# Kernel optimization log

Hardware: AMD Instinct MI355X
Metric: run time of the kernel (lower is better)

Reference implementation:

```python
import jax, jax.numpy as jnp
import numpy as np

N_NODES = 50000
HEADS = 4
NEG_SLOPE = 0.2


def _gat_conv(x, src, dst, W, a_src, a_dst, b):
    """PyG GATConv (concat=True, add_self_loops already applied to src/dst).
    x: [N, F_in], W: [F_in, H*C], a_src/a_dst: [H, C], b: [H*C]."""
    N = x.shape[0]
    HC = W.shape[1]
    C = HC // HEADS
    h = (x @ W).reshape(N, HEADS, C)                       # [N, H, C]
    alpha_s = (h * a_src[None]).sum(-1)                    # [N, H]
    alpha_d = (h * a_dst[None]).sum(-1)                    # [N, H]
    e = jax.nn.leaky_relu(alpha_s[src] + alpha_d[dst], NEG_SLOPE)  # [E, H]
    # segment softmax over incoming edges of each destination node
    m = jax.ops.segment_max(e, dst, num_segments=N)        # [N, H]
    ex = jnp.exp(e - m[dst])
    denom = jax.ops.segment_sum(ex, dst, num_segments=N)   # [N, H]
    alpha = ex / (denom[dst] + 1e-16)                      # [E, H]
    msg = h[src] * alpha[:, :, None]                       # [E, H, C]
    out = jax.ops.segment_sum(msg, dst, num_segments=N)    # [N, H, C]
    return out.reshape(N, HC) + b


def _glorot(key, shape, fan):
    lim = float(np.sqrt(6.0 / fan))
    return jax.random.uniform(key, shape, jnp.float32, -lim, lim)


def setup_inputs() -> dict:
    key = jax.random.key(0)
    ks = jax.random.split(key, 16)
    N, E, F_in, Hid, Out = N_NODES, 800000, 128, 256, 256
    x = jax.random.normal(ks[0], (N, F_in), jnp.float32)
    edge_index = jax.random.randint(ks[1], (2, E), 0, N, jnp.int64)
    C1, C2, C3 = Hid // HEADS, Hid // HEADS, Out // HEADS
    d = {"x": x, "edge_index": edge_index}
    dims = [(F_in, HEADS * C1, C1), (Hid, HEADS * C2, C2), (Hid, HEADS * C3, C3)]
    for i, (fi, fo, c) in enumerate(dims, 1):
        d[f"W{i}"] = _glorot(ks[3 * i], (fi, fo), fi + fo)
        d[f"a_src{i}"] = _glorot(ks[3 * i + 1], (HEADS, c), HEADS * c)
        d[f"a_dst{i}"] = _glorot(ks[3 * i + 2], (HEADS, c), HEADS * c)
        d[f"b{i}"] = jnp.zeros((fo,), jnp.float32)
    return d


def reference(x, edge_index, W1, a_src1, a_dst1, b1, W2, a_src2, a_dst2, b2, W3, a_src3, a_dst3, b3):
    N = x.shape[0]
    loops = jnp.arange(N, dtype=edge_index.dtype)
    src = jnp.concatenate([edge_index[0], loops])  # PyG add_self_loops=True
    dst = jnp.concatenate([edge_index[1], loops])
    h = _gat_conv(x, src, dst, W1, a_src1, a_dst1, b1)
    h = jax.nn.relu(h)  # dropout inert in eval mode
    h = _gat_conv(h, src, dst, W2, a_src2, a_dst2, b2)
    h = jax.nn.relu(h)
    return _gat_conv(h, src, dst, W3, a_src3, a_dst3, b3)
```

## Files before the change

### kernel.cpp

```cpp
#include <hip/hip_runtime.h>
#include <hip/hip_bf16.h>

typedef unsigned short u16;
typedef __attribute__((ext_vector_type(8))) short short8;
typedef __attribute__((ext_vector_type(4))) float f32x4;

#define HC 256
#define NHEAD 4

__device__ __forceinline__ u16 f2b_rne(float v) {
  __hip_bfloat16 b = __float2bfloat16(v);
  union { __hip_bfloat16 b; u16 u; } cv; cv.b = b; return cv.u;
}

__global__ void convert_w(const float* __restrict__ W, u16* __restrict__ Wth,
                          u16* __restrict__ Wtl, int K) {
  int id = blockIdx.x * 256 + threadIdx.x;
  if (id >= K * 256) return;
  int k = id >> 8, n = id & 255;
  float v = W[id];
  unsigned bits = __float_as_uint(v);
  u16 hi = (u16)(bits >> 16);
  float hf = __uint_as_float((unsigned)hi << 16);
  u16 lo = f2b_rne(v - hf);
  Wth[n * K + k] = hi;
  Wtl[n * K + k] = lo;
}

#define GBM 128
#define GBN 128
#define GBK 64

__global__ __launch_bounds__(256, 2) void gemm_mfma(
    const float* __restrict__ A, const u16* __restrict__ Bth,
    const u16* __restrict__ Btl, float* __restrict__ C, int M, int K) {
  __shared__ u16 AH[128 * 64], AL[128 * 64], BH[128 * 64], BL[128 * 64];
  const int tid = threadIdx.x;
  const int lane = tid & 63;
  const int wave = tid >> 6;
  const int wm = (wave & 1) * 64;
  const int wn = (wave >> 1) * 64;
  const int bm = blockIdx.x * GBM;
  const int bn = blockIdx.y * GBN;

  const int srow = tid >> 1;
  const int skh  = (tid & 1) * 32;

  f32x4 acc[4][4] = {};

  const int agm = (bm + srow < M) ? (bm + srow) : (M - 1);

  for (int bk = 0; bk < K; bk += GBK) {
    float4 a0[4], a1[4];
    const float* arow = A + (size_t)agm * K + bk + skh;
#pragma unroll
    for (int u = 0; u < 4; ++u) {
      a0[u] = ((const float4*)arow)[2 * u];
      a1[u] = ((const float4*)arow)[2 * u + 1];
    }
    short8 sbh[4], sbl[4];
    const u16* bhrow = Bth + (size_t)(bn + srow) * K + bk + skh;
    const u16* blrow = Btl + (size_t)(bn + srow) * K + bk + skh;
#pragma unroll
    for (int u = 0; u < 4; ++u) {
      sbh[u] = *(const short8*)(bhrow + 8 * u);
      sbl[u] = *(const short8*)(blrow + 8 * u);
    }
    __syncthreads();
#pragma unroll
    for (int u = 0; u < 4; ++u) {
      int idx = (srow * 64 + skh + u * 8) ^ ((srow & 7) << 3);
      float va[8] = {a0[u].x, a0[u].y, a0[u].z, a0[u].w,
                     a1[u].x, a1[u].y, a1[u].z, a1[u].w};
      short8 hi, lo;
#pragma unroll
      for (int j = 0; j < 8; ++j) {
        unsigned bits = __float_as_uint(va[j]);
        u16 h = (u16)(bits >> 16);
        float hf = __uint_as_float((unsigned)h << 16);
        u16 l = f2b_rne(va[j] - hf);
        ((short*)&hi)[j] = (short)h;
        ((short*)&lo)[j] = (short)l;
      }
      *(short8*)&AH[idx] = hi;
      *(short8*)&AL[idx] = lo;
      *(short8*)&BH[idx] = sbh[u];
      *(short8*)&BL[idx] = sbl[u];
    }
    __syncthreads();
#pragma unroll
    for (int ks = 0; ks < 2; ++ks) {
      const int k0 = ks * 32 + (lane >> 4) * 8;
      short8 fah[4], fal[4], fbh[4], fbl[4];
#pragma unroll
      for (int mt = 0; mt < 4; ++mt) {
        int r = wm + mt * 16 + (lane & 15);
        int idx = (r * 64 + k0) ^ ((r & 7) << 3);
        fah[mt] = *(const short8*)&AH[idx];
        fal[mt] = *(const short8*)&AL[idx];
      }
#pragma unroll
      for (int nt = 0; nt < 4; ++nt) {
        int r = wn + nt * 16 + (lane & 15);
        int idx = (r * 64 + k0) ^ ((r & 7) << 3);
        fbh[nt] = *(const short8*)&BH[idx];
        fbl[nt] = *(const short8*)&BL[idx];
      }
#pragma unroll
      for (int mt = 0; mt < 4; ++mt)
#pragma unroll
        for (int nt = 0; nt < 4; ++nt) {
          acc[mt][nt] = __builtin_amdgcn_mfma_f32_16x16x32_bf16(
              fbh[nt], fah[mt], acc[mt][nt], 0, 0, 0);
          acc[mt][nt] = __builtin_amdgcn_mfma_f32_16x16x32_bf16(
              fbh[nt], fal[mt], acc[mt][nt], 0, 0, 0);
          acc[mt][nt] = __builtin_amdgcn_mfma_f32_16x16x32_bf16(
              fbl[nt], fah[mt], acc[mt][nt], 0, 0, 0);
        }
    }
  }
#pragma unroll
  for (int mt = 0; mt < 4; ++mt) {
    int row = bm + wm + mt * 16 + (lane & 15);
    if (row < M) {
      float* cp = C + (size_t)row * HC + bn + wn + (lane >> 4) * 4;
#pragma unroll
      for (int nt = 0; nt < 4; ++nt)
        *(f32x4*)(cp + nt * 16) = acc[mt][nt];
    }
  }
}

__global__ __launch_bounds__(256) void alpha_kernel(
    const float* __restrict__ h, const float* __restrict__ a_src,
    const float* __restrict__ a_dst, float* __restrict__ as_g,
    float* __restrict__ ad_g, int N) {
  const int wave = threadIdx.x >> 6;
  const int lane = threadIdx.x & 63;
  const int n = blockIdx.x * 4 + wave;
  if (n >= N) return;
  float4 hv = ((const float4*)h)[(size_t)n * 64 + lane];
  float4 s4 = ((const float4*)a_src)[lane];
  float4 d4 = ((const float4*)a_dst)[lane];
  float ps = hv.x * s4.x + hv.y * s4.y + hv.z * s4.z + hv.w * s4.w;
  float pd = hv.x * d4.x + hv.y * d4.y + hv.z * d4.z + hv.w * d4.w;
#pragma unroll
  for (int off = 1; off < 16; off <<= 1) {
    ps += __shfl_xor(ps, off);
    pd += __shfl_xor(pd, off);
  }
  if ((lane & 15) == 0) {
    int head = lane >> 4;
    as_g[n * NHEAD + head] = ps;
    ad_g[n * NHEAD + head] = pd;
  }
}

__device__ __forceinline__ float comp4(float4 v, int i) {
  return (i == 0) ? v.x : (i == 1) ? v.y : (i == 2) ? v.z : v.w;
}

__global__ __launch_bounds__(256) void aggregate_kernel(
    const float* __restrict__ h, const float* __restrict__ as_g,
    const float* __restrict__ ad_g, const int* __restrict__ row_ptr,
    const int* __restrict__ csr_src, const float* __restrict__ bias,
    float* __restrict__ out, int relu_flag, int N) {
  const int wave = threadIdx.x >> 6;
  const int lane = threadIdx.x & 63;
  const int n = blockIdx.x * 4 + wave;
  if (n >= N) return;
  const int head = lane >> 4;
  const float4* __restrict__ h4 = (const float4*)h;
  const float4* __restrict__ as4 = (const float4*)as_g;

  const int beg = row_ptr[n];
  const int end = row_ptr[n + 1];

  float4 m4 = make_float4(-1e30f, -1e30f, -1e30f, -1e30f);
  for (int j = beg + lane; j < end; j += 64) {
    float4 a = as4[csr_src[j]];
    m4.x = fmaxf(m4.x, a.x); m4.y = fmaxf(m4.y, a.y);
    m4.z = fmaxf(m4.z, a.z); m4.w = fmaxf(m4.w, a.w);
  }
#pragma unroll
  for (int off = 32; off > 0; off >>= 1) {
    m4.x = fmaxf(m4.x, __shfl_xor(m4.x, off));
    m4.y = fmaxf(m4.y, __shfl_xor(m4.y, off));
    m4.z = fmaxf(m4.z, __shfl_xor(m4.z, off));
    m4.w = fmaxf(m4.w, __shfl_xor(m4.w, off));
  }
  const float ad = comp4(((const float4*)ad_g)[n], head);
  float mm = ad + comp4(m4, head);
  mm = (mm >= 0.f) ? mm : 0.2f * mm;

  float l = 0.f;
  float4 acc = make_float4(0.f, 0.f, 0.f, 0.f);
  for (int j0 = beg; j0 < end; j0 += 8) {
    int s[8];
    float ae[8];
    float4 hv[8];
#pragma unroll
    for (int u = 0; u < 8; ++u) {
      int j = j0 + u;
      s[u] = csr_src[(j < end) ? j : (end - 1)];
    }
#pragma unroll
    for (int u = 0; u < 8; ++u) ae[u] = as_g[s[u] * NHEAD + head];
#pragma unroll
    for (int u = 0; u < 8; ++u) hv[u] = h4[(size_t)s[u] * 64 + lane];
#pragma unroll
    for (int u = 0; u < 8; ++u) {
      float e = ae[u] + ad;
      e = (e >= 0.f) ? e : 0.2f * e;
      float p = __expf(e - mm);
      p = (j0 + u < end) ? p : 0.f;
      l += p;
      acc.x = fmaf(p, hv[u].x, acc.x);
      acc.y = fmaf(p, hv[u].y, acc.y);
      acc.z = fmaf(p, hv[u].z, acc.z);
      acc.w = fmaf(p, hv[u].w, acc.w);
    }
  }
  const float inv = 1.f / (l + 1e-16f);
  float4 b4 = ((const float4*)bias)[lane];
  float4 o;
  o.x = acc.x * inv + b4.x; o.y = acc.y * inv + b4.y;
  o.z = acc.z * inv + b4.z; o.w = acc.w * inv + b4.w;
  if (relu_flag) {
    o.x = fmaxf(o.x, 0.f); o.y = fmaxf(o.y, 0.f);
    o.z = fmaxf(o.z, 0.f); o.w = fmaxf(o.w, 0.f);
  }
  ((float4*)out)[(size_t)n * 64 + lane] = o;
}

__global__ void detect_kernel(const int* __restrict__ ei32, int* flag) {
  const int t = threadIdx.x;
  int bad = 0;
#pragma unroll
  for (int r = 0; r < 4; ++r) {
    int i = r * 64 + t;
    if (ei32[2 * i + 1] != 0) bad = 1;
  }
#pragma unroll
  for (int off = 32; off > 0; off >>= 1) bad |= __shfl_down(bad, off);
  if (t == 0) *flag = bad ? 0 : 1;
}

__device__ inline void edge_pair(const int* __restrict__ ei32,
                                 const long long* __restrict__ ei64, int is64,
                                 int e, int E, int& src, int& dst) {
  if (e < E) {
    if (is64) { src = (int)ei64[e]; dst = (int)ei64[(size_t)E + e]; }
    else      { src = ei32[e];      dst = ei32[(size_t)E + e]; }
  } else {
    src = dst = e - E;
  }
}

__global__ void count_kernel(const int* __restrict__ ei32, const int* __restrict__ flag,
                             int* __restrict__ cnt, int E, int Nn) {
  int e = blockIdx.x * blockDim.x + threadIdx.x;
  if (e >= E + Nn) return;
  int is64 = *flag;
  int src, dst;
  edge_pair(ei32, (const long long*)ei32, is64, e, E, src, dst);
  atomicAdd(&cnt[dst], 1);
}

__global__ void scatter_kernel(const int* __restrict__ ei32, const int* __restrict__ flag,
                               int* __restrict__ cursor, int* __restrict__ csr_src,
                               int E, int Nn) {
  int e = blockIdx.x * blockDim.x + threadIdx.x;
  if (e >= E + Nn) return;
  int is64 = *flag;
  int src, dst;
  edge_pair(ei32, (const long long*)ei32, is64, e, E, src, dst);
  int pos = atomicAdd(&cursor[dst], 1);
  csr_src[pos] = src;
}

__global__ __launch_bounds__(256) void scan_blocks(
    const int* __restrict__ cnt, int* __restrict__ local,
    int* __restrict__ partials, int Nn) {
  __shared__ int swave[4];
  const int t = threadIdx.x, lane = t & 63, w = t >> 6;
  const int idx = blockIdx.x * 256 + t;
  int v = (idx < Nn) ? cnt[idx] : 0;
  int x = v;
#pragma unroll
  for (int off = 1; off < 64; off <<= 1) {
    int y = __shfl_up(x, off);
    if (lane >= off) x += y;
  }
  if (lane == 63) swave[w] = x;
  __syncthreads();
  int wofs = 0;
#pragma unroll
  for (int i = 0; i < 3; ++i) wofs += (i < w) ? swave[i] : 0;
  if (idx < Nn) local[idx] = wofs + x - v;
  if (t == 255) partials[blockIdx.x] = wofs + x;
}

__global__ __launch_bounds__(256) void scan_partials(
    int* __restrict__ partials, int nb, int* __restrict__ total_out) {
  __shared__ int swave[4];
  const int t = threadIdx.x, lane = t & 63, w = t >> 6;
  int v = (t < nb) ? partials[t] : 0;
  int x = v;
#pragma unroll
  for (int off = 1; off < 64; off <<= 1) {
    int y = __shfl_up(x, off);
    if (lane >= off) x += y;
  }
  if (lane == 63) swave[w] = x;
  __syncthreads();
  int wofs = 0;
#pragma unroll
  for (int i = 0; i < 3; ++i) wofs += (i < w) ? swave[i] : 0;
  int excl = wofs + x - v;
  if (t < nb) partials[t] = excl;
  if (t == nb - 1) *total_out = excl + v;
}

__global__ void add_offsets(const int* __restrict__ local,
                            const int* __restrict__ partials,
                            int* __restrict__ row_ptr, int* __restrict__ cursor,
                            int Nn) {
  const int idx = blockIdx.x * 256 + threadIdx.x;
  if (idx < Nn) {
    int v = local[idx] + partials[blockIdx.x];
    row_ptr[idx] = v;
    cursor[idx] = v;
  }
}

static inline size_t align_up(size_t v) { return (v + 255) & ~(size_t)255; }

extern "C" void kernel_launch(void* const* d_in, const int* in_sizes, int n_in,
                              void* d_out, int out_size, void* d_ws, size_t ws_size,
                              hipStream_t stream) {
  const float* x      = (const float*)d_in[0];
  const int*   ei32   = (const int*)d_in[1];
  const float* W1     = (const float*)d_in[2];
  const float* asrc1  = (const float*)d_in[3];
  const float* adst1  = (const float*)d_in[4];
  const float* b1     = (const float*)d_in[5];
  const float* W2     = (const float*)d_in[6];
  const float* asrc2  = (const float*)d_in[7];
  const float* adst2  = (const float*)d_in[8];
  const float* b2     = (const float*)d_in[9];
  const float* W3     = (const float*)d_in[10];
  const float* asrc3  = (const float*)d_in[11];
  const float* adst3  = (const float*)d_in[12];
  const float* b3     = (const float*)d_in[13];

  const int N = in_sizes[0] / 128;
  const int E = in_sizes[1] / 2;
  const int ET = E + N;
  float* out = (float*)d_out;
  const int nb = (N + 255) / 256;

  char* w = (char*)d_ws;
  float* H       = (float*)w; w += align_up((size_t)N * HC * sizeof(float));
  float* AS      = (float*)w; w += align_up((size_t)N * NHEAD * sizeof(float));
  float* AD      = (float*)w; w += align_up((size_t)N * NHEAD * sizeof(float));
  int*   cnt     = (int*)w;   w += align_up((size_t)N * sizeof(int));
  int*   local   = (int*)w;   w += align_up((size_t)N * sizeof(int));
  int*   row_ptr = (int*)w;   w += align_up((size_t)(N + 1) * sizeof(int));
  int*   cursor  = (int*)w;   w += align_up((size_t)(N + 1) * sizeof(int));
  int*   parts   = (int*)w;   w += align_up(256 * sizeof(int));
  int*   csr_src = (int*)w;   w += align_up((size_t)ET * sizeof(int));
  u16*   Wth     = (u16*)w;   w += align_up((size_t)256 * 256 * sizeof(u16));
  u16*   Wtl     = (u16*)w;   w += align_up((size_t)256 * 256 * sizeof(u16));
  int*   flag    = (int*)w;   w += align_up(sizeof(int));

  hipMemsetAsync(cnt, 0, (size_t)N * sizeof(int), stream);
  detect_kernel<<<1, 64, 0, stream>>>(ei32, flag);
  count_kernel<<<(ET + 255) / 256, 256, 0, stream>>>(ei32, flag, cnt, E, N);
  scan_blocks<<<nb, 256, 0, stream>>>(cnt, local, parts, N);
  scan_partials<<<1, 256, 0, stream>>>(parts, nb, row_ptr + N);
  add_offsets<<<nb, 256, 0, stream>>>(local, parts, row_ptr, cursor, N);
  scatter_kernel<<<(ET + 255) / 256, 256, 0, stream>>>(ei32, flag, cursor, csr_src, E, N);

  const dim3 gemm_grid((N + GBM - 1) / GBM, HC / GBN);
  const int ablk = (N + 3) / 4;

  convert_w<<<(128 * 256 + 255) / 256, 256, 0, stream>>>(W1, Wth, Wtl, 128);
  gemm_mfma<<<gemm_grid, 256, 0, stream>>>(x, Wth, Wtl, H, N, 128);
  alpha_kernel<<<ablk, 256, 0, stream>>>(H, asrc1, adst1, AS, AD, N);
  aggregate_kernel<<<ablk, 256, 0, stream>>>(H, AS, AD, row_ptr, csr_src, b1, out, 1, N);

  convert_w<<<(256 * 256 + 255) / 256, 256, 0, stream>>>(W2, Wth, Wtl, 256);
  gemm_mfma<<<gemm_grid, 256, 0, stream>>>(out, Wth, Wtl, H, N, 256);
  alpha_kernel<<<ablk, 256, 0, stream>>>(H, asrc2, adst2, AS, AD, N);
  aggregate_kernel<<<ablk, 256, 0, stream>>>(H, AS, AD, row_ptr, csr_src, b2, out, 1, N);

  convert_w<<<(256 * 256 + 255) / 256, 256, 0, stream>>>(W3, Wth, Wtl, 256);
  gemm_mfma<<<gemm_grid, 256, 0, stream>>>(out, Wth, Wtl, H, N, 256);
  alpha_kernel<<<ablk, 256, 0, stream>>>(H, asrc3, adst3, AS, AD, N);
  aggregate_kernel<<<ablk, 256, 0, stream>>>(H, AS, AD, row_ptr, csr_src, b3, out, 0, N);
}
```

Before: 611.8 us.

## Split softmax edge weights into separate kernel and use two waves per node

Moves the per-edge exp/leaky-relu softmax weight computation and normalizer into a new edge_weights kernel that writes weights to a workspace buffer. The aggregation kernel then uses two waves per destination node, each covering alternating chunks of 8 edges, and combines their partial sums through shared memory. This targets latency in the gather loop by doubling the memory-level parallelism per node. In exchange it adds an extra kernel launch per layer and an extra write and read of an E×4 float weight buffer, plus a block-wide synchronisation.

```diff
diff --git a/kernel.cpp b/kernel.cpp
--- a/kernel.cpp
+++ b/kernel.cpp
@@ -160,19 +160,17 @@
   return (i == 0) ? v.x : (i == 1) ? v.y : (i == 2) ? v.z : v.w;
 }
 
-__global__ __launch_bounds__(256) void aggregate_kernel(
-    const float* __restrict__ h, const float* __restrict__ as_g,
-    const float* __restrict__ ad_g, const int* __restrict__ row_ptr,
-    const int* __restrict__ csr_src, const float* __restrict__ bias,
-    float* __restrict__ out, int relu_flag, int N) {
+__global__ __launch_bounds__(256) void edge_weights(
+    const float* __restrict__ as_g, const float* __restrict__ ad_g,
+    const int* __restrict__ row_ptr, const int* __restrict__ csr_src,
+    float* __restrict__ w_buf, float* __restrict__ inv_l, int N) {
   const int wave = threadIdx.x >> 6;
   const int lane = threadIdx.x & 63;
   const int n = blockIdx.x * 4 + wave;
   if (n >= N) return;
   const int head = lane >> 4;
-  const float4* __restrict__ h4 = (const float4*)h;
+  const int sub = lane & 15;
   const float4* __restrict__ as4 = (const float4*)as_g;
-
   const int beg = row_ptr[n];
   const int end = row_ptr[n + 1];
 
@@ -193,44 +191,82 @@
   float mm = ad + comp4(m4, head);
   mm = (mm >= 0.f) ? mm : 0.2f * mm;
 
-  float l = 0.f;
+  float lsum = 0.f;
+  for (int j0 = beg; j0 < end; j0 += 16) {
+    int j = j0 + sub;
+    int jc = (j < end) ? j : (end - 1);
+    int s = csr_src[jc];
+    float e = as_g[s * NHEAD + head] + ad;
+    e = (e >= 0.f) ? e : 0.2f * e;
+    float w = __expf(e - mm);
+    w_buf[(size_t)jc * NHEAD + head] = w;
+    lsum += (j < end) ? w : 0.f;
+  }
+#pragma unroll
+  for (int off = 1; off < 16; off <<= 1) lsum += __shfl_xor(lsum, off);
+  if (sub == 0) inv_l[n * NHEAD + head] = 1.f / (lsum + 1e-16f);
+}
+
+__global__ __launch_bounds__(512, 4) void aggregate_kernel(
+    const float* __restrict__ h, const float* __restrict__ w_buf,
+    const float* __restrict__ inv_l, const int* __restrict__ row_ptr,
+    const int* __restrict__ csr_src, const float* __restrict__ bias,
+    float* __restrict__ out, int relu_flag, int N) {
+  __shared__ float4 lacc[4][64];
+  const int wave = threadIdx.x >> 6;
+  const int lane = threadIdx.x & 63;
+  const int p = wave >> 1;
+  const int q = wave & 1;
+  const int n = blockIdx.x * 4 + p;
+  const int nc = (n < N) ? n : (N - 1);
+  const int head = lane >> 4;
+  const float4* __restrict__ h4 = (const float4*)h;
+
+  const int beg = row_ptr[nc];
+  const int end = row_ptr[nc + 1];
+
   float4 acc = make_float4(0.f, 0.f, 0.f, 0.f);
-  for (int j0 = beg; j0 < end; j0 += 8) {
-    int s[8];
-    float ae[8];
+  for (int j0 = beg + q * 8; j0 < end; j0 += 16) {
+    int jc[8];
+    float wv[8];
     float4 hv[8];
 #pragma unroll
     for (int u = 0; u < 8; ++u) {
       int j = j0 + u;
-      s[u] = csr_src[(j < end) ? j : (end - 1)];
-    }
-#pragma unroll
-    for (int u = 0; u < 8; ++u) ae[u] = as_g[s[u] * NHEAD + head];
-#pragma unroll
-    for (int u = 0; u < 8; ++u) hv[u] = h4[(size_t)s[u] * 64 + lane];
+      jc[u] = (j < end) ? j : (end - 1);
+    }
+    int sv[8];
+#pragma unroll
+    for (int u = 0; u < 8; ++u) sv[u] = csr_src[jc[u]];
+#pragma unroll
+    for (int u = 0; u < 8; ++u) wv[u] = w_buf[(size_t)jc[u] * NHEAD + head];
+#pragma unroll
+    for (int u = 0; u < 8; ++u) hv[u] = h4[(size_t)sv[u] * 64 + lane];
 #pragma unroll
     for (int u = 0; u < 8; ++u) {
-      float e = ae[u] + ad;
-      e = (e >= 0.f) ? e : 0.2f * e;
-      float p = __expf(e - mm);
-      p = (j0 + u < end) ? p : 0.f;
-      l += p;
-      acc.x = fmaf(p, hv[u].x, acc.x);
-      acc.y = fmaf(p, hv[u].y, acc.y);
-      acc.z = fmaf(p, hv[u].z, acc.z);
-      acc.w = fmaf(p, hv[u].w, acc.w);
-    }
-  }
-  const float inv = 1.f / (l + 1e-16f);
-  float4 b4 = ((const float4*)bias)[lane];
-  float4 o;
-  o.x = acc.x * inv + b4.x; o.y = acc.y * inv + b4.y;
-  o.z = acc.z * inv + b4.z; o.w = acc.w * inv + b4.w;
-  if (relu_flag) {
-    o.x = fmaxf(o.x, 0.f); o.y = fmaxf(o.y, 0.f);
-    o.z = fmaxf(o.z, 0.f); o.w = fmaxf(o.w, 0.f);
-  }
-  ((float4*)out)[(size_t)n * 64 + lane] = o;
+      float wm = (j0 + u < end) ? wv[u] : 0.f;
+      acc.x = fmaf(wm, hv[u].x, acc.x);
+      acc.y = fmaf(wm, hv[u].y, acc.y);
+      acc.z = fmaf(wm, hv[u].z, acc.z);
+      acc.w = fmaf(wm, hv[u].w, acc.w);
+    }
+  }
+  if (q == 1) lacc[p][lane] = acc;
+  __syncthreads();
+  if (q == 0 && n < N) {
+    float4 a2 = lacc[p][lane];
+    acc.x += a2.x; acc.y += a2.y; acc.z += a2.z; acc.w += a2.w;
+    const float il = inv_l[n * NHEAD + head];
+    float4 b4 = ((const float4*)bias)[lane];
+    float4 o;
+    o.x = acc.x * il + b4.x; o.y = acc.y * il + b4.y;
+    o.z = acc.z * il + b4.z; o.w = acc.w * il + b4.w;
+    if (relu_flag) {
+      o.x = fmaxf(o.x, 0.f); o.y = fmaxf(o.y, 0.f);
+      o.z = fmaxf(o.z, 0.f); o.w = fmaxf(o.w, 0.f);
+    }
+    ((float4*)out)[(size_t)n * 64 + lane] = o;
+  }
 }
 
 __global__ void detect_kernel(const int* __restrict__ ei32, int* flag) {
@@ -364,6 +400,8 @@
   float* H       = (float*)w; w += align_up((size_t)N * HC * sizeof(float));
   float* AS      = (float*)w; w += align_up((size_t)N * NHEAD * sizeof(float));
   float* AD      = (float*)w; w += align_up((size_t)N * NHEAD * sizeof(float));
+  float* INVL    = (float*)w; w += align_up((size_t)N * NHEAD * sizeof(float));
+  float* WBUF    = (float*)w; w += align_up((size_t)ET * NHEAD * sizeof(float));
   int*   cnt     = (int*)w;   w += align_up((size_t)N * sizeof(int));
   int*   local   = (int*)w;   w += align_up((size_t)N * sizeof(int));
   int*   row_ptr = (int*)w;   w += align_up((size_t)(N + 1) * sizeof(int));
@@ -388,15 +426,18 @@
   convert_w<<<(128 * 256 + 255) / 256, 256, 0, stream>>>(W1, Wth, Wtl, 128);
   gemm_mfma<<<gemm_grid, 256, 0, stream>>>(x, Wth, Wtl, H, N, 128);
   alpha_kernel<<<ablk, 256, 0, stream>>>(H, asrc1, adst1, AS, AD, N);
-  aggregate_kernel<<<ablk, 256, 0, stream>>>(H, AS, AD, row_ptr, csr_src, b1, out, 1, N);
+  edge_weights<<<ablk, 256, 0, stream>>>(AS, AD, row_ptr, csr_src, WBUF, INVL, N);
+  aggregate_kernel<<<ablk, 512, 0, stream>>>(H, WBUF, INVL, row_ptr, csr_src, b1, out, 1, N);
 
   convert_w<<<(256 * 256 + 255) / 256, 256, 0, stream>>>(W2, Wth, Wtl, 256);
   gemm_mfma<<<gemm_grid, 256, 0, stream>>>(out, Wth, Wtl, H, N, 256);
   alpha_kernel<<<ablk, 256, 0, stream>>>(H, asrc2, adst2, AS, AD, N);
-  aggregate_kernel<<<ablk, 256, 0, stream>>>(H, AS, AD, row_ptr, csr_src, b2, out, 1, N);
+  edge_weights<<<ablk, 256, 0, stream>>>(AS, AD, row_ptr, csr_src, WBUF, INVL, N);
+  aggregate_kernel<<<ablk, 512, 0, stream>>>(H, WBUF, INVL, row_ptr, csr_src, b2, out, 1, N);
 
   convert_w<<<(256 * 256 + 255) / 256, 256, 0, stream>>>(W3, Wth, Wtl, 256);
   gemm_mfma<<<gemm_grid, 256, 0, stream>>>(out, Wth, Wtl, H, N, 256);
   alpha_kernel<<<ablk, 256, 0, stream>>>(H, asrc3, adst3, AS, AD, N);
-  aggregate_kernel<<<ablk, 256, 0, stream>>>(H, AS, AD, row_ptr, csr_src, b3, out, 0, N);
-}
+  edge_weights<<<ablk, 256, 0, stream>>>(AS, AD, row_ptr, csr_src, WBUF, INVL, N);
+  aggregate_kernel<<<ablk, 512, 0, stream>>>(H, WBUF, INVL, row_ptr, csr_src, b3, out, 0, N);
+}
```

After: 664.5 us. 1.09x slower.
